# Performance work log

Measured on AMD Instinct MI355X. Metric: run time of the kernel, lower is better.

## Reference

```python
import jax, jax.numpy as jnp
import numpy as np

K = 32  # k-th nearest neighbor (excluding self), matches KDistanceDetector(k=32)


def setup_inputs() -> dict:
    key = jax.random.key(0)
    B, D = 16384, 128
    images = jax.random.normal(key, (B, D), dtype=jnp.float32)
    return {"images": images}


def reference(images):
    # model is identity: vision_features = images, shape [B, D]
    x = images
    # torch.cdist p=2 with mm path: sq dists via gram matrix
    sq_norms = jnp.sum(x * x, axis=1)                      # [B]
    sq = sq_norms[:, None] + sq_norms[None, :] - 2.0 * (x @ x.T)  # [B, B]
    sq = jnp.maximum(sq, 0.0)
    B = x.shape[0]
    # Mask out the diagonal (self-distance). Original removes it and views
    # [B, B-1]; setting it to +inf before sorting yields the identical k-th
    # smallest value (inf sorts last), and keeps sqrt grads clean.
    diag = jnp.eye(B, dtype=bool)
    sq = jnp.where(diag, jnp.inf, sq)
    d = jnp.sqrt(sq)                                       # [B, B]
    a = jnp.sort(d, axis=1)                                # full per-row sort, as in original
    return a[:, K]                                         # [B]
```

## Files before the change

### kernel.cpp

```cpp
#include <hip/hip_runtime.h>


typedef unsigned short u16;
typedef unsigned int   u32;
typedef __attribute__((ext_vector_type(8))) u16    ushort8;
typedef __attribute__((ext_vector_type(8))) __bf16 bf16x8;
typedef __attribute__((ext_vector_type(4))) float  f32x4;
typedef __attribute__((ext_vector_type(4))) u32    u32x4;

#define NB   16384
#define ND   128
#define NSEG 32
#define SCAP 12
#define NTH  33
#define ZWH  (-2.62f)
#define NEGF (-3.0e38f)
#define POSF ( 3.0e38f)

#define OFF_X    ((size_t)0)
#define OFF_NORM (OFF_X    + (size_t)NB * ND * 2)
#define OFF_TACC (OFF_NORM + (size_t)NB * 4)
#define OFF_XBAR (OFF_TACC + (size_t)NB * 4)
#define OFF_SCAL (OFF_XBAR + 512)
#define OFF_CNTS (OFF_SCAL + 256)
#define OFF_CAND (OFF_CNTS + (size_t)NB * NSEG * 4)

static __device__ __forceinline__ u16 f2bf(float f) {
  u32 u = __float_as_uint(f);
  u32 r = u + 0x7FFFu + ((u >> 16) & 1u);
  return (u16)(r >> 16);
}
static __device__ __forceinline__ float bf2f(u16 h) {
  return __uint_as_float(((u32)h) << 16);
}

#if defined(__has_builtin)
#if __has_builtin(__builtin_amdgcn_global_load_lds)
#define HAVE_GLDS 1
#endif
#endif

static __device__ __forceinline__ void stage16(const u16* gsrc_lane,
                                               u16* lds_base, int l) {
#ifdef HAVE_GLDS
  __builtin_amdgcn_global_load_lds(
      (const __attribute__((address_space(1))) void*)gsrc_lane,
      (__attribute__((address_space(3))) void*)lds_base, 16, 0, 0);
#else
  *(ushort8*)(lds_base + l * 8) = *(const ushort8*)gsrc_lane;
#endif
}
static __device__ __forceinline__ void stage4(const float* gsrc_lane,
                                              float* lds_base, int l) {
#ifdef HAVE_GLDS
  __builtin_amdgcn_global_load_lds(
      (const __attribute__((address_space(1))) void*)gsrc_lane,
      (__attribute__((address_space(3))) void*)lds_base, 4, 0, 0);
#else
  lds_base[l] = *gsrc_lane;
#endif
}

__global__ void k_prep(const float* __restrict__ x, u16* __restrict__ X,
                       float* __restrict__ norms, float* xbar, float* scal) {
  if (blockIdx.x == 0) {
    int tt = threadIdx.x;
    if (tt < 128) xbar[tt] = 0.f;
    if (tt < 2)   scal[tt] = 0.f;
  }
  int w = threadIdx.x >> 6, l = threadIdx.x & 63;
  int r = blockIdx.x * 4 + w;
  const float2* xr2 = (const float2*)(x + (size_t)r * ND);
  float2 a = xr2[l];
  u16 h0 = f2bf(a.x), h1 = f2bf(a.y);
  float b0 = bf2f(h0), b1 = bf2f(h1);
  float n = b0 * b0 + b1 * b1;
#pragma unroll
  for (int off = 1; off < 64; off <<= 1) n += __shfl_xor(n, off, 64);
  *(u32*)(X + (size_t)r * ND + 2 * l) = (u32)h0 | ((u32)h1 << 16);
  if (l == 0) norms[r] = n;
}

__global__ void k_stats(const u16* __restrict__ X, const float* __restrict__ norms,
                        float* xbar, float* scal) {
  __shared__ float xs[2][128];
  __shared__ float red1[256], red2[256];
  int t = threadIdx.x, col = t & 127, half = t >> 7;
  int rbase = blockIdx.x * 256 + half * 128;
  float acc = 0.f;
  for (int rr = 0; rr < 128; ++rr)
    acc += bf2f(X[(size_t)(rbase + rr) * ND + col]);
  xs[half][col] = acc;
  float ln = norms[blockIdx.x * 256 + t];
  red1[t] = ln; red2[t] = ln * ln;
  __syncthreads();
  for (int s = 128; s > 0; s >>= 1) {
    if (t < s) { red1[t] += red1[t + s]; red2[t] += red2[t + s]; }
    __syncthreads();
  }
  if (t == 0) { atomicAdd(&scal[0], red1[0]); atomicAdd(&scal[1], red2[0]); }
  if (t < 128) atomicAdd(&xbar[t], xs[0][t] + xs[1][t]);
}

__global__ void k_thresh(const u16* __restrict__ X, const float* __restrict__ norms,
                         const float* __restrict__ xbar, const float* __restrict__ scal,
                         float* __restrict__ tacc) {
  __shared__ float xb[128];
  int t = threadIdx.x;
  if (t < 128) xb[t] = xbar[t] * (1.0f / NB);
  __syncthreads();
  int r = blockIdx.x * 256 + t;
  float n = norms[r];
  const u16* xr = X + (size_t)r * ND;
  float dot = 0.f;
#pragma unroll
  for (int c8 = 0; c8 < 16; ++c8) {
    ushort8 v = *(const ushort8*)(xr + c8 * 8);
#pragma unroll
    for (int j = 0; j < 8; ++j) dot += bf2f(v[j]) * xb[c8 * 8 + j];
  }
  float nbar = scal[0] * (1.0f / NB);
  float Vn = fmaxf(scal[1] * (1.0f / NB) - nbar * nbar, 0.f);
  float m = n + nbar - 2.f * dot;
  float v = Vn + 4.f * n * (nbar / ND);
  float nu = 2.f * m * m / v;
  float cc = v / (2.f * m);
  float a1 = 2.f / (9.f * nu);
  float inner = 1.f - a1 + ZWH * sqrtf(a1);
  float tsq = cc * nu * inner * inner * inner;
  tacc[r] = 0.5f * (n - tsq);
}

#define FILTER_TILE(DGC)                                                      \
  _Pragma("unroll") for (int i = 0; i < 4; ++i) {                             \
    _Pragma("unroll") for (int j = 0; j < 4; ++j) {                           \
      _Pragma("unroll") for (int v = 0; v < 4; ++v) {                         \
        float val = acc[i][j][v] - nch4[i][v];                                \
        bool p = (val >= tj[j]);                                              \
        if (DGC) p = p && ((c0 + wc * 64 + i * 16 + lq * 4 + v) != rj[j]);    \
        if (p) {                                                              \
          u32 c = cnt4[j];                                                    \
          if (c < SCAP) cands[segb[j] + c] = val;                             \
          cnt4[j] = c + 1;                                                    \
        }                                                                     \
      }                                                                       \
    }                                                                         \
  }

__global__ __launch_bounds__(256, 2) void k_gram(
    const u16* __restrict__ X, const float* __restrict__ norms,
    const float* __restrict__ tacc, u32* __restrict__ counts,
    float* __restrict__ cands) {
  __shared__ u16 ldsA[2][32 * 512];
  __shared__ __align__(16) float nchs[2][128];
  const int bid = blockIdx.x;
  const int logical = (bid & 7) * 64 + (bid >> 3);
  const int q = logical >> 7, strip = logical & 127;
  const int r0 = strip * 128;
  const int t = threadIdx.x, w = t >> 6, l = t & 63;
  const int wr = w & 1, wc = w >> 1;
  const int lm = l & 15, lq = l >> 4;
  const int koff = lq * 8;

  bf16x8 bfrag[4][4];
#pragma unroll
  for (int k = 0; k < 4; ++k)
#pragma unroll
    for (int j = 0; j < 4; ++j)
      bfrag[k][j] = __builtin_bit_cast(bf16x8, *(const ushort8*)(
          X + (size_t)(r0 + (wr * 4 + j) * 16 + lm) * ND + k * 32 + koff));

  int rj[4]; float tj[4]; u32 cnt4[4]; u32 segb[4];
#pragma unroll
  for (int j = 0; j < 4; ++j) {
    rj[j] = r0 + (wr * 4 + j) * 16 + lm;
    tj[j] = tacc[rj[j]];
    cnt4[j] = 0;
    segb[j] = (u32)(rj[j] * NSEG + q * 8 + wc * 4 + lq) * SCAP;
  }

  {
    const int c0 = q * 4096;
#pragma unroll
    for (int s = 0; s < 8; ++s) {
      int g = w * 8 + s;
      stage16(X + (size_t)(c0 + (g & 7) * 16 + lm) * ND + (g >> 3) * 32 + koff,
              &ldsA[0][g * 512], l);
    }
    if (w < 2) stage4(norms + c0 + w * 64 + l, &nchs[0][w * 64], l);
  }
  __syncthreads();

  for (int it = 0; it < 32; ++it) {
    const int cur = it & 1;
    const int c0 = q * 4096 + it * 128;
    if (it + 1 < 32) {
      const int c1 = c0 + 128;
      u16* dstA = ldsA[cur ^ 1];
#pragma unroll
      for (int s = 0; s < 8; ++s) {
        int g = w * 8 + s;
        stage16(X + (size_t)(c1 + (g & 7) * 16 + lm) * ND + (g >> 3) * 32 + koff,
                &dstA[g * 512], l);
      }
      if (w < 2) stage4(norms + c1 + w * 64 + l, &nchs[cur ^ 1][w * 64], l);
    }
    __builtin_amdgcn_sched_barrier(0);

    f32x4 acc[4][4];
#pragma unroll
    for (int i = 0; i < 4; ++i)
#pragma unroll
      for (int j = 0; j < 4; ++j) acc[i][j] = (f32x4){0.f, 0.f, 0.f, 0.f};

    const u16* srcA = ldsA[cur];
#pragma unroll
    for (int k = 0; k < 4; ++k) {
      bf16x8 af[4];
#pragma unroll
      for (int i = 0; i < 4; ++i)
        af[i] = __builtin_bit_cast(bf16x8,
                 *(const ushort8*)(&srcA[(k * 8 + wc * 4 + i) * 512 + l * 8]));
#pragma unroll
      for (int i = 0; i < 4; ++i)
#pragma unroll
        for (int j = 0; j < 4; ++j)
          acc[i][j] = __builtin_amdgcn_mfma_f32_16x16x32_bf16(af[i], bfrag[k][j], acc[i][j], 0, 0, 0);
    }

    f32x4 nch4[4];
#pragma unroll
    for (int i = 0; i < 4; ++i) {
      nch4[i] = *(const f32x4*)(&nchs[cur][wc * 64 + i * 16 + lq * 4]);
      nch4[i] = nch4[i] * 0.5f;
    }

    if (c0 == r0) { FILTER_TILE(true) } else { FILTER_TILE(false) }

    __syncthreads();
  }
#pragma unroll
  for (int j = 0; j < 4; ++j)
    counts[rj[j] * NSEG + q * 8 + wc * 4 + lq] = cnt4[j];
}

__global__ void k_select(const u32* __restrict__ counts, const float* __restrict__ cands,
                         const float* __restrict__ norms, float* __restrict__ out) {
  int w = threadIdx.x >> 6, l = threadIdx.x & 63;
  int r = blockIdx.x * 4 + w;
  u32 myc = (l < NSEG) ? counts[r * NSEG + l] : 0u;
  u32 tot = myc, mx = myc;
#pragma unroll
  for (int off = 1; off < 64; off <<= 1) {
    tot += __shfl_xor(tot, off, 64);
    u32 o = (u32)__shfl_xor((int)mx, off, 64);
    mx = mx > o ? mx : o;
  }
  if (tot < NTH || mx > SCAP) return;

  const float* base = cands + (size_t)r * (NSEG * SCAP);
  float v0, v1, v2, v3, v4, v5;
#define LOADV(e, dst)                                        \
  {                                                          \
    int f = l + 64 * e;                                      \
    int sg = f / SCAP, sl = f - sg * SCAP;                   \
    u32 c = (u32)__shfl((int)myc, sg, 64);                   \
    float x = base[f];                                       \
    dst = (sl < (int)c) ? x : NEGF;                          \
  }
  LOADV(0, v0) LOADV(1, v1) LOADV(2, v2) LOADV(3, v3) LOADV(4, v4) LOADV(5, v5)
#undef LOADV

  float last = NEGF;
  for (int e = 0; e < NTH; ++e) {
    float m = fmaxf(fmaxf(fmaxf(v0, v1), fmaxf(v2, v3)), fmaxf(v4, v5));
#pragma unroll
    for (int off = 1; off < 64; off <<= 1) m = fmaxf(m, __shfl_xor(m, off, 64));
    bool mine = (v0 == m) || (v1 == m) || (v2 == m) || (v3 == m) || (v4 == m) || (v5 == m);
    unsigned long long bal = __ballot(mine);
    int owner = __ffsll(bal) - 1;
    if (l == owner) {
      if      (v0 == m) v0 = NEGF;
      else if (v1 == m) v1 = NEGF;
      else if (v2 == m) v2 = NEGF;
      else if (v3 == m) v3 = NEGF;
      else if (v4 == m) v4 = NEGF;
      else              v5 = NEGF;
    }
    last = m;
  }
  out[r] = sqrtf(fmaxf(norms[r] - 2.f * last, 0.f));
}

__global__ void k_fallback(const u32* __restrict__ counts, const u16* __restrict__ X,
                           const float* __restrict__ norms, float* __restrict__ out) {
  __shared__ float sq[NB];
  __shared__ float xr[ND];
  __shared__ float rmin[256];
  __shared__ int   ridx[256];
  __shared__ int   nbad;
  __shared__ int   badlist[256];
  int t = threadIdx.x;
  if (t == 0) nbad = 0;
  __syncthreads();
  int r = blockIdx.x * 256 + t;
  u32 tot = 0, mx = 0;
#pragma unroll
  for (int s4 = 0; s4 < 8; ++s4) {
    u32x4 c = *(const u32x4*)(counts + (size_t)r * NSEG + s4 * 4);
#pragma unroll
    for (int u = 0; u < 4; ++u) { tot += c[u]; mx = c[u] > mx ? c[u] : mx; }
  }
  if (tot < NTH || mx > SCAP) { int p = atomicAdd(&nbad, 1); badlist[p] = r; }
  __syncthreads();
  int nb = nbad;
  for (int ii = 0; ii < nb; ++ii) {
    int rr = badlist[ii];
    if (t < 128) xr[t] = bf2f(X[(size_t)rr * ND + t]);
    __syncthreads();
    float n_r = norms[rr];
    for (int jj = 0; jj < 64; ++jj) {
      int j = t + 256 * jj;
      const u16* xj = X + (size_t)j * ND;
      float dot = 0.f;
#pragma unroll
      for (int c8 = 0; c8 < 16; ++c8) {
        ushort8 vv = *(const ushort8*)(xj + c8 * 8);
#pragma unroll
        for (int u = 0; u < 8; ++u) dot += bf2f(vv[u]) * xr[c8 * 8 + u];
      }
      sq[j] = (j == rr) ? POSF : fmaxf(n_r + norms[j] - 2.f * dot, 0.f);
    }
    __syncthreads();
    float last = 0.f;
    for (int e = 0; e < NTH; ++e) {
      float lm = POSF; int li = -1;
      for (int jj = 0; jj < 64; ++jj) {
        int j = t + 256 * jj;
        float s = sq[j];
        if (s < lm) { lm = s; li = j; }
      }
      rmin[t] = lm; ridx[t] = li;
      __syncthreads();
      if (t == 0) {
        float gm = POSF; int gi = -1;
        for (int u = 0; u < 256; ++u)
          if (rmin[u] < gm) { gm = rmin[u]; gi = ridx[u]; }
        sq[gi] = POSF;
        rmin[0] = gm;
      }
      __syncthreads();
      last = rmin[0];
      __syncthreads();
    }
    if (t == 0) out[rr] = sqrtf(fmaxf(last, 0.f));
    __syncthreads();
  }
}

extern "C" void kernel_launch(void* const* d_in, const int* in_sizes, int n_in,
                              void* d_out, int out_size, void* d_ws, size_t ws_size,
                              hipStream_t stream) {
  const float* x = (const float*)d_in[0];
  float* out = (float*)d_out;
  char* ws = (char*)d_ws;
  u16*   X     = (u16*)  (ws + OFF_X);
  float* norms = (float*)(ws + OFF_NORM);
  float* tacc  = (float*)(ws + OFF_TACC);
  float* xbar  = (float*)(ws + OFF_XBAR);
  float* scal  = (float*)(ws + OFF_SCAL);
  u32*   cnts  = (u32*)  (ws + OFF_CNTS);
  float* cands = (float*)(ws + OFF_CAND);

  k_prep    <<<4096, 256, 0, stream>>>(x, X, norms, xbar, scal);
  k_stats   <<<64,   256, 0, stream>>>(X, norms, xbar, scal);
  k_thresh  <<<64,   256, 0, stream>>>(X, norms, xbar, scal, tacc);
  k_gram    <<<512,  256, 0, stream>>>(X, norms, tacc, cnts, cands);
  k_select  <<<4096, 256, 0, stream>>>(cnts, cands, norms, out);
  k_fallback<<<64,   256, 0, stream>>>(cnts, X, norms, out);
}
```

Measured before the change: 200.2 us.

## Split gram columns into 8 quarters with LDS atomic candidate buffers per row

Splits the column range of k_gram into 8 parts instead of 4, doubling the grid to 1024 blocks with three blocks per CU. It drops LDS double buffering in favour of a single buffer with syncs around staging, and replaces per-lane register counters with shared-memory atomic counters per row. Candidates are collected in LDS and flushed in one pass into 8 segments of 32 slots each. k_stats is rewritten to use vectorized loads, and k_select is adjusted to the new segment layout. The cost is lost load/compute overlap and contention on the LDS atomics, and the larger per-segment capacity changes how often rows fall back.

Result: slower. 279.5 us (+39.6%).

```diff
diff --git a/kernel.cpp b/kernel.cpp
--- a/kernel.cpp
+++ b/kernel.cpp
@@ -10,8 +10,8 @@
 
 #define NB   16384
 #define ND   128
-#define NSEG 32
-#define SCAP 12
+#define NSEG 8
+#define SCAP 32
 #define NTH  33
 #define ZWH  (-2.62f)
 #define NEGF (-3.0e38f)
@@ -83,23 +83,34 @@
 
 __global__ void k_stats(const u16* __restrict__ X, const float* __restrict__ norms,
                         float* xbar, float* scal) {
-  __shared__ float xs[2][128];
+  __shared__ float xs[16][128];
   __shared__ float red1[256], red2[256];
-  int t = threadIdx.x, col = t & 127, half = t >> 7;
-  int rbase = blockIdx.x * 256 + half * 128;
-  float acc = 0.f;
-  for (int rr = 0; rr < 128; ++rr)
-    acc += bf2f(X[(size_t)(rbase + rr) * ND + col]);
-  xs[half][col] = acc;
-  float ln = norms[blockIdx.x * 256 + t];
+  int t = threadIdx.x;
+  int cg = t & 15;
+  int rs = t >> 4;
+  int rbase = blockIdx.x * 256;
+  float s[8] = {0.f, 0.f, 0.f, 0.f, 0.f, 0.f, 0.f, 0.f};
+  for (int rr = 0; rr < 16; ++rr) {
+    int row = rbase + rs + rr * 16;
+    ushort8 v = *(const ushort8*)(X + (size_t)row * ND + cg * 8);
+#pragma unroll
+    for (int u = 0; u < 8; ++u) s[u] += bf2f(v[u]);
+  }
+#pragma unroll
+  for (int u = 0; u < 8; ++u) xs[rs][cg * 8 + u] = s[u];
+  float ln = norms[rbase + t];
   red1[t] = ln; red2[t] = ln * ln;
   __syncthreads();
-  for (int s = 128; s > 0; s >>= 1) {
-    if (t < s) { red1[t] += red1[t + s]; red2[t] += red2[t + s]; }
+  if (t < 128) {
+    float a = 0.f;
+    for (int rsub = 0; rsub < 16; ++rsub) a += xs[rsub][t];
+    atomicAdd(&xbar[t], a);
+  }
+  for (int st = 128; st > 0; st >>= 1) {
+    if (t < st) { red1[t] += red1[t + st]; red2[t] += red2[t + st]; }
     __syncthreads();
   }
   if (t == 0) { atomicAdd(&scal[0], red1[0]); atomicAdd(&scal[1], red2[0]); }
-  if (t < 128) atomicAdd(&xbar[t], xs[0][t] + xs[1][t]);
 }
 
 __global__ void k_thresh(const u16* __restrict__ X, const float* __restrict__ norms,
@@ -131,32 +142,19 @@
   tacc[r] = 0.5f * (n - tsq);
 }
 
-#define FILTER_TILE(DGC)                                                      \
-  _Pragma("unroll") for (int i = 0; i < 4; ++i) {                             \
-    _Pragma("unroll") for (int j = 0; j < 4; ++j) {                           \
-      _Pragma("unroll") for (int v = 0; v < 4; ++v) {                         \
-        float val = acc[i][j][v] - nch4[i][v];                                \
-        bool p = (val >= tj[j]);                                              \
-        if (DGC) p = p && ((c0 + wc * 64 + i * 16 + lq * 4 + v) != rj[j]);    \
-        if (p) {                                                              \
-          u32 c = cnt4[j];                                                    \
-          if (c < SCAP) cands[segb[j] + c] = val;                             \
-          cnt4[j] = c + 1;                                                    \
-        }                                                                     \
-      }                                                                       \
-    }                                                                         \
-  }
-
-__global__ __launch_bounds__(256, 2) void k_gram(
+__global__ __launch_bounds__(256, 3) void k_gram(
     const u16* __restrict__ X, const float* __restrict__ norms,
     const float* __restrict__ tacc, u32* __restrict__ counts,
     float* __restrict__ cands) {
-  __shared__ u16 ldsA[2][32 * 512];
-  __shared__ __align__(16) float nchs[2][128];
+  __shared__ u16 ldsA[32 * 512];
+  __shared__ __align__(16) float nchs[128];
+  __shared__ u32 cntL[128];
+  __shared__ float candL[128 * SCAP];
   const int bid = blockIdx.x;
-  const int logical = (bid & 7) * 64 + (bid >> 3);
+  const int logical = (bid & 7) * 128 + (bid >> 3);
   const int q = logical >> 7, strip = logical & 127;
   const int r0 = strip * 128;
+  const int cbase = q * 2048;
   const int t = threadIdx.x, w = t >> 6, l = t & 63;
   const int wr = w & 1, wc = w >> 1;
   const int lm = l & 15, lq = l >> 4;
@@ -170,85 +168,105 @@
       bfrag[k][j] = __builtin_bit_cast(bf16x8, *(const ushort8*)(
           X + (size_t)(r0 + (wr * 4 + j) * 16 + lm) * ND + k * 32 + koff));
 
-  int rj[4]; float tj[4]; u32 cnt4[4]; u32 segb[4];
+  int rj[4]; float tj[4];
 #pragma unroll
   for (int j = 0; j < 4; ++j) {
     rj[j] = r0 + (wr * 4 + j) * 16 + lm;
     tj[j] = tacc[rj[j]];
-    cnt4[j] = 0;
-    segb[j] = (u32)(rj[j] * NSEG + q * 8 + wc * 4 + lq) * SCAP;
-  }
-
+  }
+  if (t < 128) cntL[t] = 0u;
   {
-    const int c0 = q * 4096;
 #pragma unroll
     for (int s = 0; s < 8; ++s) {
       int g = w * 8 + s;
-      stage16(X + (size_t)(c0 + (g & 7) * 16 + lm) * ND + (g >> 3) * 32 + koff,
-              &ldsA[0][g * 512], l);
-    }
-    if (w < 2) stage4(norms + c0 + w * 64 + l, &nchs[0][w * 64], l);
-  }
-  __syncthreads();
-
-  for (int it = 0; it < 32; ++it) {
-    const int cur = it & 1;
-    const int c0 = q * 4096 + it * 128;
-    if (it + 1 < 32) {
+      stage16(X + (size_t)(cbase + (g & 7) * 16 + lm) * ND + (g >> 3) * 32 + koff,
+              &ldsA[g * 512], l);
+    }
+    if (w < 2) stage4(norms + cbase + w * 64 + l, &nchs[w * 64], l);
+  }
+  __syncthreads();
+
+  for (int it = 0; it < 16; ++it) {
+    const int c0 = cbase + it * 128;
+    f32x4 acc[4][4];
+#pragma unroll
+    for (int i = 0; i < 4; ++i)
+#pragma unroll
+      for (int j = 0; j < 4; ++j) acc[i][j] = (f32x4){0.f, 0.f, 0.f, 0.f};
+
+#pragma unroll
+    for (int k = 0; k < 4; ++k) {
+      bf16x8 af[4];
+#pragma unroll
+      for (int i = 0; i < 4; ++i)
+        af[i] = __builtin_bit_cast(bf16x8,
+                 *(const ushort8*)(&ldsA[(k * 8 + wc * 4 + i) * 512 + l * 8]));
+#pragma unroll
+      for (int i = 0; i < 4; ++i)
+#pragma unroll
+        for (int j = 0; j < 4; ++j)
+          acc[i][j] = __builtin_amdgcn_mfma_f32_16x16x32_bf16(af[i], bfrag[k][j], acc[i][j], 0, 0, 0);
+    }
+
+    f32x4 nch4[4];
+#pragma unroll
+    for (int i = 0; i < 4; ++i) {
+      nch4[i] = *(const f32x4*)(&nchs[wc * 64 + i * 16 + lq * 4]);
+      nch4[i] = nch4[i] * 0.5f;
+    }
+
+    const bool dg = (c0 == r0);
+#pragma unroll
+    for (int i = 0; i < 4; ++i) {
+#pragma unroll
+      for (int j = 0; j < 4; ++j) {
+        f32x4 val = acc[i][j] - nch4[i];
+        float g01 = fmaxf(val[0], val[1]);
+        float g23 = fmaxf(val[2], val[3]);
+        if (fmaxf(g01, g23) >= tj[j]) {
+          int rloc = (wr * 4 + j) * 16 + lm;
+#pragma unroll
+          for (int v = 0; v < 4; ++v) {
+            bool p = (val[v] >= tj[j]);
+            if (dg) p = p && ((c0 + wc * 64 + i * 16 + lq * 4 + v) != rj[j]);
+            if (p) {
+              u32 pos = atomicAdd(&cntL[rloc], 1u);
+              if (pos < SCAP) candL[rloc * SCAP + pos] = val[v];
+            }
+          }
+        }
+      }
+    }
+
+    if (it + 1 < 16) {
+      __syncthreads();
       const int c1 = c0 + 128;
-      u16* dstA = ldsA[cur ^ 1];
 #pragma unroll
       for (int s = 0; s < 8; ++s) {
         int g = w * 8 + s;
         stage16(X + (size_t)(c1 + (g & 7) * 16 + lm) * ND + (g >> 3) * 32 + koff,
-                &dstA[g * 512], l);
-      }
-      if (w < 2) stage4(norms + c1 + w * 64 + l, &nchs[cur ^ 1][w * 64], l);
-    }
-    __builtin_amdgcn_sched_barrier(0);
-
-    f32x4 acc[4][4];
-#pragma unroll
-    for (int i = 0; i < 4; ++i)
-#pragma unroll
-      for (int j = 0; j < 4; ++j) acc[i][j] = (f32x4){0.f, 0.f, 0.f, 0.f};
-
-    const u16* srcA = ldsA[cur];
-#pragma unroll
-    for (int k = 0; k < 4; ++k) {
-      bf16x8 af[4];
-#pragma unroll
-      for (int i = 0; i < 4; ++i)
-        af[i] = __builtin_bit_cast(bf16x8,
-                 *(const ushort8*)(&srcA[(k * 8 + wc * 4 + i) * 512 + l * 8]));
-#pragma unroll
-      for (int i = 0; i < 4; ++i)
-#pragma unroll
-        for (int j = 0; j < 4; ++j)
-          acc[i][j] = __builtin_amdgcn_mfma_f32_16x16x32_bf16(af[i], bfrag[k][j], acc[i][j], 0, 0, 0);
-    }
-
-    f32x4 nch4[4];
-#pragma unroll
-    for (int i = 0; i < 4; ++i) {
-      nch4[i] = *(const f32x4*)(&nchs[cur][wc * 64 + i * 16 + lq * 4]);
-      nch4[i] = nch4[i] * 0.5f;
-    }
-
-    if (c0 == r0) { FILTER_TILE(true) } else { FILTER_TILE(false) }
-
-    __syncthreads();
-  }
-#pragma unroll
-  for (int j = 0; j < 4; ++j)
-    counts[rj[j] * NSEG + q * 8 + wc * 4 + lq] = cnt4[j];
+                &ldsA[g * 512], l);
+      }
+      if (w < 2) stage4(norms + c1 + w * 64 + l, &nchs[w * 64], l);
+      __syncthreads();
+    }
+  }
+
+  __syncthreads();
+  if (t < 128) counts[(size_t)(r0 + t) * NSEG + q] = cntL[t];
+#pragma unroll
+  for (int u = 0; u < 16; ++u) {
+    int idx = t + u * 256;
+    int row = idx >> 5, s = idx & 31;
+    cands[((size_t)(r0 + row) * NSEG + q) * SCAP + s] = candL[idx];
+  }
 }
 
 __global__ void k_select(const u32* __restrict__ counts, const float* __restrict__ cands,
                          const float* __restrict__ norms, float* __restrict__ out) {
   int w = threadIdx.x >> 6, l = threadIdx.x & 63;
   int r = blockIdx.x * 4 + w;
-  u32 myc = (l < NSEG) ? counts[r * NSEG + l] : 0u;
+  u32 myc = (l < NSEG) ? counts[(size_t)r * NSEG + l] : 0u;
   u32 tot = myc, mx = myc;
 #pragma unroll
   for (int off = 1; off < 64; off <<= 1) {
@@ -259,33 +277,31 @@
   if (tot < NTH || mx > SCAP) return;
 
   const float* base = cands + (size_t)r * (NSEG * SCAP);
-  float v0, v1, v2, v3, v4, v5;
+  float v0, v1, v2, v3;
 #define LOADV(e, dst)                                        \
   {                                                          \
     int f = l + 64 * e;                                      \
-    int sg = f / SCAP, sl = f - sg * SCAP;                   \
+    int sg = f >> 5, sl = f & 31;                            \
     u32 c = (u32)__shfl((int)myc, sg, 64);                   \
     float x = base[f];                                       \
     dst = (sl < (int)c) ? x : NEGF;                          \
   }
-  LOADV(0, v0) LOADV(1, v1) LOADV(2, v2) LOADV(3, v3) LOADV(4, v4) LOADV(5, v5)
+  LOADV(0, v0) LOADV(1, v1) LOADV(2, v2) LOADV(3, v3)
 #undef LOADV
 
   float last = NEGF;
   for (int e = 0; e < NTH; ++e) {
-    float m = fmaxf(fmaxf(fmaxf(v0, v1), fmaxf(v2, v3)), fmaxf(v4, v5));
+    float m = fmaxf(fmaxf(v0, v1), fmaxf(v2, v3));
 #pragma unroll
     for (int off = 1; off < 64; off <<= 1) m = fmaxf(m, __shfl_xor(m, off, 64));
-    bool mine = (v0 == m) || (v1 == m) || (v2 == m) || (v3 == m) || (v4 == m) || (v5 == m);
+    bool mine = (v0 == m) || (v1 == m) || (v2 == m) || (v3 == m);
     unsigned long long bal = __ballot(mine);
     int owner = __ffsll(bal) - 1;
     if (l == owner) {
       if      (v0 == m) v0 = NEGF;
       else if (v1 == m) v1 = NEGF;
       else if (v2 == m) v2 = NEGF;
-      else if (v3 == m) v3 = NEGF;
-      else if (v4 == m) v4 = NEGF;
-      else              v5 = NEGF;
+      else              v3 = NEGF;
     }
     last = m;
   }
@@ -306,7 +322,7 @@
   int r = blockIdx.x * 256 + t;
   u32 tot = 0, mx = 0;
 #pragma unroll
-  for (int s4 = 0; s4 < 8; ++s4) {
+  for (int s4 = 0; s4 < 2; ++s4) {
     u32x4 c = *(const u32x4*)(counts + (size_t)r * NSEG + s4 * 4);
 #pragma unroll
     for (int u = 0; u < 4; ++u) { tot += c[u]; mx = c[u] > mx ? c[u] : mx; }
@@ -375,7 +391,7 @@
   k_prep    <<<4096, 256, 0, stream>>>(x, X, norms, xbar, scal);
   k_stats   <<<64,   256, 0, stream>>>(X, norms, xbar, scal);
   k_thresh  <<<64,   256, 0, stream>>>(X, norms, xbar, scal, tacc);
-  k_gram    <<<512,  256, 0, stream>>>(X, norms, tacc, cnts, cands);
+  k_gram    <<<1024, 256, 0, stream>>>(X, norms, tacc, cnts, cands);
   k_select  <<<4096, 256, 0, stream>>>(cnts, cands, norms, out);
   k_fallback<<<64,   256, 0, stream>>>(cnts, X, norms, out);
 }
```
